# Performance work log

Measured on AMD Instinct MI355X. Metric: run time of the kernel, lower is better.

Reference implementation:

```python
import jax, jax.numpy as jnp
import numpy as np

TEMPERATURE = 0.07
EPS = 1e-12  # F.normalize eps


def _construct_labels(visual_ids, anchor_idx):
    # Faithful vectorization of the original order-dependent double loop:
    # for i < B-1: final write to labels[i] comes from pair (i, B-1)
    #   -> 1 iff ids[i]==anchor_id and ids[B-1]==anchor_id, else 0
    # for i == B-1: final write comes from pair (B-2, B-1)
    #   -> 1 iff ids[B-1]==anchor_id and ids[B-2]==anchor_id, else 0
    B = visual_ids.shape[0]
    anchor_id = visual_ids[anchor_idx]
    same = visual_ids == anchor_id  # [B] bool
    labels = jnp.where(same & same[B - 1], 1, 0).astype(jnp.int32)
    labels = labels.at[B - 1].set((same[B - 1] & same[B - 2]).astype(jnp.int32))
    return labels


def setup_inputs() -> dict:
    key = jax.random.key(0)
    k1, k2 = jax.random.split(key)
    visual_feat = jax.random.normal(k1, (8192, 512), dtype=jnp.float32)
    visual_ids = jax.random.randint(k2, (8192,), 0, 1024, dtype=jnp.int64 if jax.config.jax_enable_x64 else jnp.int32)
    anchor_idx = 3
    return {"visual_feat": visual_feat, "visual_ids": visual_ids, "anchor_idx": anchor_idx}


def reference(visual_feat, visual_ids, anchor_idx):
    # L2 normalize rows (F.normalize: x / max(||x||, eps))
    norm = jnp.sqrt(jnp.sum(visual_feat * visual_feat, axis=1, keepdims=True))
    f = visual_feat / jnp.maximum(norm, EPS)
    sim = jnp.matmul(f, f.T) / TEMPERATURE  # [B, B]
    labels = _construct_labels(visual_ids, anchor_idx)  # [B] int in {0,1}
    logp = jax.nn.log_softmax(sim, axis=-1)  # [B, B]
    picked = jnp.take_along_axis(logp, labels[:, None], axis=1)[:, 0]
    loss = -jnp.mean(picked)
    return loss
```

## Files before the change

kernel.cpp:

```cpp
#include <hip/hip_runtime.h>


typedef int i32x8 __attribute__((ext_vector_type(8)));
typedef float f32x4 __attribute__((ext_vector_type(4)));

#define B_N 8192
#define D_K 512
#define ROWB 512
#define INVT 14.285714285714286f
#define SCALE_LOG2 20.609929155556622f

#if defined(__has_builtin) && __has_builtin(__builtin_amdgcn_exp2f)
#define FAST_EXP2(x) __builtin_amdgcn_exp2f(x)
#else
#define FAST_EXP2(x) exp2f(x)
#endif

union FragU {
  int4 h[2];
  i32x8 v;
};

static __device__ __forceinline__ void load16_to_lds(const void* g, void* l) {
  __builtin_amdgcn_global_load_lds(
      (const __attribute__((address_space(1))) unsigned int*)g,
      (__attribute__((address_space(3))) unsigned int*)l, 16, 0, 0);
}

static __device__ __forceinline__ void bar_nodrain() {
  __builtin_amdgcn_sched_barrier(0);
  asm volatile("" ::: "memory");
  __builtin_amdgcn_s_barrier();
  asm volatile("" ::: "memory");
  __builtin_amdgcn_sched_barrier(0);
}

#define VM_WAIT(N) asm volatile("s_waitcnt vmcnt(" #N ")" ::: "memory")

__global__ __launch_bounds__(256)
void norm_kernel(const float* __restrict__ x,
                 unsigned char* __restrict__ fQ,
                 float* __restrict__ Z) {
  const int row = blockIdx.x * 4 + (threadIdx.x >> 6);
  const int lane = threadIdx.x & 63;
  const float4* xr = (const float4*)(x + (size_t)row * D_K);
  float4 a = xr[2 * lane];
  float4 b = xr[2 * lane + 1];
  float s = a.x * a.x + a.y * a.y + a.z * a.z + a.w * a.w +
            b.x * b.x + b.y * b.y + b.z * b.z + b.w * b.w;
#pragma unroll
  for (int off = 1; off < 64; off <<= 1) s += __shfl_xor(s, off);
  const float inv = 1.0f / fmaxf(sqrtf(s), 1e-12f);
  int lo = 0, hi = 0;
  lo = __builtin_amdgcn_cvt_pk_fp8_f32(a.x * inv, a.y * inv, lo, false);
  lo = __builtin_amdgcn_cvt_pk_fp8_f32(a.z * inv, a.w * inv, lo, true);
  hi = __builtin_amdgcn_cvt_pk_fp8_f32(b.x * inv, b.y * inv, hi, false);
  hi = __builtin_amdgcn_cvt_pk_fp8_f32(b.z * inv, b.w * inv, hi, true);
  int2 p; p.x = lo; p.y = hi;
  ((int2*)(fQ + (size_t)row * ROWB))[lane] = p;
  if (lane == 0) Z[row] = 0.0f;
}

__global__ __launch_bounds__(256, 2)
void sim_kernel(const unsigned char* __restrict__ fQ,
                float* __restrict__ Z, float* __restrict__ T01,
                float* __restrict__ D) {
  __shared__ unsigned char ldsA[3 * 128 * 128];
  __shared__ unsigned char ldsB[2 * 128 * 128];

  const int tid = threadIdx.x;
  const int lane = tid & 63;
  const int w = tid >> 6;
  const int wm = w & 1;
  const int wn = w >> 1;
  const int bx = blockIdx.x, by = blockIdx.y;
  const int b = by & 7;
  const int I = (by < 8) ? bx : (63 - bx);
  const int Jfirst = I + ((b - I) & 7);
  if (Jfirst > 63) return;
  const int I0 = I * 128;

  const int srow = lane >> 3;
  const int sb = lane & 7;
  const int su = sb ^ srow;
  const int sg = 2 * (su & 3) + (su >> 2);
  const size_t sOff = (size_t)srow * ROWB + sg * 16;

  const int fr = lane & 15;
  const int q = lane >> 4;
  const int swz = fr & 7;

  const int raRow = (wm * 64 + fr) * 128;
  const int rbRow = (wn * 64 + fr) * 128;
  const int off0 = (q ^ swz) * 16;
  const int off1 = ((q + 4) ^ swz) * 16;

  FragU u3[4];
  {
    const unsigned char* aReg =
        fQ + (size_t)(I0 + wm * 64 + fr) * ROWB + 3 * 128 + q * 32;
#pragma unroll
    for (int m = 0; m < 4; ++m) {
      const unsigned char* p = aReg + (size_t)(m * 16) * ROWB;
      u3[m].h[0] = *(const int4*)(p);
      u3[m].h[1] = *(const int4*)(p + 16);
    }
  }
#pragma unroll
  for (int m = 0; m < 4; ++m) asm volatile("" ::"v"(u3[m].v));

#pragma unroll
  for (int kk = 0; kk < 3; ++kk) {
    const unsigned char* gA = fQ + (size_t)(I0 + w * 32) * ROWB + kk * 128 + sOff;
    unsigned char* lA = ldsA + kk * (128 * 128) + (w * 32) * 128;
#pragma unroll
    for (int rr = 0; rr < 32; rr += 8)
      load16_to_lds(gA + (size_t)rr * ROWB, lA + rr * 128);
  }

  int curOff = 0;
  {
    const unsigned char* gB =
        fQ + (size_t)(Jfirst * 128 + w * 32) * ROWB + sOff;
    unsigned char* lB = ldsB + (w * 32) * 128;
#pragma unroll
    for (int rr = 0; rr < 32; rr += 8)
      load16_to_lds(gB + (size_t)rr * ROWB, lB + rr * 128);
  }

  float Zp[4][4];
#pragma unroll
  for (int m = 0; m < 4; ++m)
#pragma unroll
    for (int r = 0; r < 4; ++r) Zp[m][r] = 0.0f;

  f32x4 acc[4][4];

#pragma unroll 1
  for (int J = Jfirst; J < 64; J += 8) {
    const int J0 = J * 128;
#pragma unroll
    for (int m = 0; m < 4; ++m)
#pragma unroll
      for (int n = 0; n < 4; ++n) acc[m][n] = (f32x4){0.f, 0.f, 0.f, 0.f};

#pragma unroll 1
    for (int kk = 0; kk < 3; ++kk) {
      {
        const unsigned char* gB =
            fQ + (size_t)(J0 + w * 32) * ROWB + (kk + 1) * 128 + sOff;
        unsigned char* lB = ldsB + (curOff ^ 16384) + (w * 32) * 128;
#pragma unroll
        for (int rr = 0; rr < 32; rr += 8)
          load16_to_lds(gB + (size_t)rr * ROWB, lB + rr * 128);
      }
      VM_WAIT(4);
      bar_nodrain();

      const unsigned char* raBase = ldsA + kk * (128 * 128) + raRow;
      const unsigned char* rbBase = ldsB + curOff + rbRow;
      i32x8 bv[4];
#pragma unroll
      for (int n = 0; n < 4; ++n) {
        const unsigned char* rb = rbBase + n * 16 * 128;
        FragU u;
        u.h[0] = *(const int4*)(rb + off0);
        u.h[1] = *(const int4*)(rb + off1);
        bv[n] = u.v;
      }
      __builtin_amdgcn_s_setprio(1);
#pragma unroll
      for (int mh = 0; mh < 2; ++mh) {
        i32x8 av[2];
#pragma unroll
        for (int m = 0; m < 2; ++m) {
          const unsigned char* ra = raBase + (mh * 2 + m) * 16 * 128;
          FragU u;
          u.h[0] = *(const int4*)(ra + off0);
          u.h[1] = *(const int4*)(ra + off1);
          av[m] = u.v;
        }
#pragma unroll
        for (int m = 0; m < 2; ++m)
#pragma unroll
          for (int n = 0; n < 4; ++n)
            acc[mh * 2 + m][n] = __builtin_amdgcn_mfma_scale_f32_16x16x128_f8f6f4(
                av[m], bv[n], acc[mh * 2 + m][n], 0, 0, 0, 127, 0, 127);
      }
      __builtin_amdgcn_s_setprio(0);
      bar_nodrain();
      curOff ^= 16384;
    }

    const bool hasNext = (J + 8) < 64;
    if (hasNext) {
      const unsigned char* gB =
          fQ + (size_t)((J + 8) * 128 + w * 32) * ROWB + sOff;
      unsigned char* lB = ldsB + (curOff ^ 16384) + (w * 32) * 128;
#pragma unroll
      for (int rr = 0; rr < 32; rr += 8)
        load16_to_lds(gB + (size_t)rr * ROWB, lB + rr * 128);
      VM_WAIT(4);
    } else {
      VM_WAIT(0);
    }
    bar_nodrain();
    {
      const unsigned char* rbBase = ldsB + curOff + rbRow;
      i32x8 bv[4];
#pragma unroll
      for (int n = 0; n < 4; ++n) {
        const unsigned char* rb = rbBase + n * 16 * 128;
        FragU u;
        u.h[0] = *(const int4*)(rb + off0);
        u.h[1] = *(const int4*)(rb + off1);
        bv[n] = u.v;
      }
      __builtin_amdgcn_s_setprio(1);
#pragma unroll
      for (int m = 0; m < 4; ++m)
#pragma unroll
        for (int n = 0; n < 4; ++n)
          acc[m][n] = __builtin_amdgcn_mfma_scale_f32_16x16x128_f8f6f4(
              u3[m].v, bv[n], acc[m][n], 0, 0, 0, 127, 0, 127);
      __builtin_amdgcn_s_setprio(0);
    }
    curOff ^= 16384;

    if (I == 0 && wm == 0) {
      if (q == 0) {
#pragma unroll
        for (int n = 0; n < 4; ++n) {
          const int col = J0 + wn * 64 + n * 16 + fr;
          T01[col * 2 + 0] = acc[0][n][0] * INVT;
          T01[col * 2 + 1] = acc[0][n][1] * INVT;
        }
      }
    }

    if (J == I) {
#pragma unroll
      for (int m = 0; m < 4; ++m)
#pragma unroll
        for (int n = 0; n < 4; ++n) {
          const int col = J0 + wn * 64 + n * 16 + fr;
#pragma unroll
          for (int r = 0; r < 4; ++r) {
            const int row = I0 + wm * 64 + m * 16 + q * 4 + r;
            if (row == col) D[row] = acc[m][n][r];
          }
        }
    }

    const bool offd = (J != I);
#pragma unroll
    for (int n = 0; n < 4; ++n) {
      float cs = 0.0f;
#pragma unroll
      for (int m = 0; m < 4; ++m)
#pragma unroll
        for (int r = 0; r < 4; ++r) {
          const float e = FAST_EXP2((acc[m][n][r] - 1.0f) * SCALE_LOG2);
          Zp[m][r] += e;
          cs += e;
        }
      if (offd) {
        cs += __shfl_xor(cs, 16);
        cs += __shfl_xor(cs, 32);
        if (q == 0) atomicAdd(&Z[J0 + wn * 64 + n * 16 + fr], cs);
      }
    }

    bar_nodrain();
  }

#pragma unroll
  for (int m = 0; m < 4; ++m)
#pragma unroll
    for (int r = 0; r < 4; ++r) {
      float v = Zp[m][r];
      v += __shfl_xor(v, 1);
      v += __shfl_xor(v, 2);
      v += __shfl_xor(v, 4);
      v += __shfl_xor(v, 8);
      if (fr == 0) atomicAdd(&Z[I0 + wm * 64 + m * 16 + q * 4 + r], v);
    }
}

__global__ __launch_bounds__(1024)
void finalize_kernel(const float* __restrict__ Z,
                     const float* __restrict__ T01,
                     const float* __restrict__ D,
                     const int* __restrict__ ids,
                     const int* __restrict__ anchor,
                     float* __restrict__ out) {
  __shared__ float red[1024];
  const int t = threadIdx.x;
  const int anchor_id = ids[anchor[0]];
  const int sameLast = (ids[B_N - 1] == anchor_id);
  const int samePrev = (ids[B_N - 2] == anchor_id);
  int i[8], id[8];
  float z[8], d[8], t0[8], t1[8];
#pragma unroll
  for (int u = 0; u < 8; ++u) {
    i[u] = u * 1024 + t;
    z[u] = Z[i[u]];
    d[u] = D[i[u]];
    t0[u] = T01[i[u] * 2 + 0];
    t1[u] = T01[i[u] * 2 + 1];
    id[u] = ids[i[u]];
  }
  float sum = 0.0f;
#pragma unroll
  for (int u = 0; u < 8; ++u) {
    const int same_i = (id[u] == anchor_id);
    const int lab =
        (i[u] < B_N - 1) ? (same_i & sameLast) : (sameLast & samePrev);
    const float tt = lab ? t1[u] : t0[u];
    const float Zc = z[u] - FAST_EXP2((d[u] - 1.0f) * SCALE_LOG2) + 1.0f;
    sum += tt - (INVT + logf(Zc));
  }
  red[t] = sum;
  __syncthreads();
  for (int off = 512; off > 0; off >>= 1) {
    if (t < off) red[t] += red[t + off];
    __syncthreads();
  }
  if (t == 0) out[0] = -red[0] / (float)B_N;
}

extern "C" void kernel_launch(void* const* d_in, const int* in_sizes, int n_in,
                              void* d_out, int out_size, void* d_ws, size_t ws_size,
                              hipStream_t stream) {
  const float* x = (const float*)d_in[0];
  const int* ids = (const int*)d_in[1];
  const int* anchor = (const int*)d_in[2];
  float* out = (float*)d_out;

  unsigned char* fQ = (unsigned char*)d_ws;
  float* Z = (float*)((char*)d_ws + (size_t)B_N * ROWB);
  float* T01 = Z + B_N;
  float* D = T01 + 2 * B_N;

  norm_kernel<<<B_N / 4, 256, 0, stream>>>(x, fQ, Z);
  sim_kernel<<<dim3(32, 16), 256, 0, stream>>>(fQ, Z, T01, D);
  finalize_kernel<<<1, 1024, 0, stream>>>(Z, T01, D, ids, anchor, out);
}
```

Before: 107.4 us.

## Keep three A K-slices in registers and shrink A LDS to one slice

Three of the four 128-wide K slices of the A tile now live in registers for the whole block, and only K slice 0 is staged in LDS. This cuts LDS from 80KB to 48KB and removes the A-side LDS reads for those slices. The k-loop is unrolled, and B fragments are now loaded per column and consumed right away instead of being buffered as a full set of four. The cost is much higher VGPR pressure (48 extra 8-dword fragments per thread), which risks spills or lower occupancy under launch_bounds(256,2).

```diff
diff --git a/kernel.cpp b/kernel.cpp
--- a/kernel.cpp
+++ b/kernel.cpp
@@ -65,7 +65,7 @@
 void sim_kernel(const unsigned char* __restrict__ fQ,
                 float* __restrict__ Z, float* __restrict__ T01,
                 float* __restrict__ D) {
-  __shared__ unsigned char ldsA[3 * 128 * 128];
+  __shared__ unsigned char ldsA0[128 * 128];
   __shared__ unsigned char ldsB[2 * 128 * 128];
 
   const int tid = threadIdx.x;
@@ -95,24 +95,28 @@
   const int off0 = (q ^ swz) * 16;
   const int off1 = ((q + 4) ^ swz) * 16;
 
-  FragU u3[4];
+  FragU uA[3][4];
   {
-    const unsigned char* aReg =
-        fQ + (size_t)(I0 + wm * 64 + fr) * ROWB + 3 * 128 + q * 32;
-#pragma unroll
-    for (int m = 0; m < 4; ++m) {
-      const unsigned char* p = aReg + (size_t)(m * 16) * ROWB;
-      u3[m].h[0] = *(const int4*)(p);
-      u3[m].h[1] = *(const int4*)(p + 16);
-    }
-  }
-#pragma unroll
-  for (int m = 0; m < 4; ++m) asm volatile("" ::"v"(u3[m].v));
-
-#pragma unroll
-  for (int kk = 0; kk < 3; ++kk) {
-    const unsigned char* gA = fQ + (size_t)(I0 + w * 32) * ROWB + kk * 128 + sOff;
-    unsigned char* lA = ldsA + kk * (128 * 128) + (w * 32) * 128;
+    const unsigned char* aBase =
+        fQ + (size_t)(I0 + wm * 64 + fr) * ROWB + q * 32;
+#pragma unroll
+    for (int k = 0; k < 3; ++k) {
+#pragma unroll
+      for (int m = 0; m < 4; ++m) {
+        const unsigned char* p = aBase + (size_t)(m * 16) * ROWB + (k + 1) * 128;
+        uA[k][m].h[0] = *(const int4*)(p);
+        uA[k][m].h[1] = *(const int4*)(p + 16);
+      }
+    }
+  }
+#pragma unroll
+  for (int k = 0; k < 3; ++k)
+#pragma unroll
+    for (int m = 0; m < 4; ++m) asm volatile("" ::"v"(uA[k][m].v));
+
+  {
+    const unsigned char* gA = fQ + (size_t)(I0 + w * 32) * ROWB + sOff;
+    unsigned char* lA = ldsA0 + (w * 32) * 128;
 #pragma unroll
     for (int rr = 0; rr < 32; rr += 8)
       load16_to_lds(gA + (size_t)rr * ROWB, lA + rr * 128);
@@ -144,11 +148,10 @@
 #pragma unroll
       for (int n = 0; n < 4; ++n) acc[m][n] = (f32x4){0.f, 0.f, 0.f, 0.f};
 
-#pragma unroll 1
-    for (int kk = 0; kk < 3; ++kk) {
+    {
       {
         const unsigned char* gB =
-            fQ + (size_t)(J0 + w * 32) * ROWB + (kk + 1) * 128 + sOff;
+            fQ + (size_t)(J0 + w * 32) * ROWB + 1 * 128 + sOff;
         unsigned char* lB = ldsB + (curOff ^ 16384) + (w * 32) * 128;
 #pragma unroll
         for (int rr = 0; rr < 32; rr += 8)
@@ -157,35 +160,58 @@
       VM_WAIT(4);
       bar_nodrain();
 
-      const unsigned char* raBase = ldsA + kk * (128 * 128) + raRow;
       const unsigned char* rbBase = ldsB + curOff + rbRow;
-      i32x8 bv[4];
+      i32x8 av[4];
+#pragma unroll
+      for (int m = 0; m < 4; ++m) {
+        const unsigned char* ra = ldsA0 + raRow + m * 16 * 128;
+        FragU u;
+        u.h[0] = *(const int4*)(ra + off0);
+        u.h[1] = *(const int4*)(ra + off1);
+        av[m] = u.v;
+      }
+      __builtin_amdgcn_s_setprio(1);
 #pragma unroll
       for (int n = 0; n < 4; ++n) {
         const unsigned char* rb = rbBase + n * 16 * 128;
-        FragU u;
-        u.h[0] = *(const int4*)(rb + off0);
-        u.h[1] = *(const int4*)(rb + off1);
-        bv[n] = u.v;
-      }
+        FragU ub;
+        ub.h[0] = *(const int4*)(rb + off0);
+        ub.h[1] = *(const int4*)(rb + off1);
+#pragma unroll
+        for (int m = 0; m < 4; ++m)
+          acc[m][n] = __builtin_amdgcn_mfma_scale_f32_16x16x128_f8f6f4(
+              av[m], ub.v, acc[m][n], 0, 0, 0, 127, 0, 127);
+      }
+      __builtin_amdgcn_s_setprio(0);
+      bar_nodrain();
+      curOff ^= 16384;
+    }
+
+#pragma unroll
+    for (int k = 0; k < 2; ++k) {
+      {
+        const unsigned char* gB =
+            fQ + (size_t)(J0 + w * 32) * ROWB + (k + 2) * 128 + sOff;
+        unsigned char* lB = ldsB + (curOff ^ 16384) + (w * 32) * 128;
+#pragma unroll
+        for (int rr = 0; rr < 32; rr += 8)
+          load16_to_lds(gB + (size_t)rr * ROWB, lB + rr * 128);
+      }
+      VM_WAIT(4);
+      bar_nodrain();
+
+      const unsigned char* rbBase = ldsB + curOff + rbRow;
       __builtin_amdgcn_s_setprio(1);
 #pragma unroll
-      for (int mh = 0; mh < 2; ++mh) {
-        i32x8 av[2];
-#pragma unroll
-        for (int m = 0; m < 2; ++m) {
-          const unsigned char* ra = raBase + (mh * 2 + m) * 16 * 128;
-          FragU u;
-          u.h[0] = *(const int4*)(ra + off0);
-          u.h[1] = *(const int4*)(ra + off1);
-          av[m] = u.v;
-        }
-#pragma unroll
-        for (int m = 0; m < 2; ++m)
-#pragma unroll
-          for (int n = 0; n < 4; ++n)
-            acc[mh * 2 + m][n] = __builtin_amdgcn_mfma_scale_f32_16x16x128_f8f6f4(
-                av[m], bv[n], acc[mh * 2 + m][n], 0, 0, 0, 127, 0, 127);
+      for (int n = 0; n < 4; ++n) {
+        const unsigned char* rb = rbBase + n * 16 * 128;
+        FragU ub;
+        ub.h[0] = *(const int4*)(rb + off0);
+        ub.h[1] = *(const int4*)(rb + off1);
+#pragma unroll
+        for (int m = 0; m < 4; ++m)
+          acc[m][n] = __builtin_amdgcn_mfma_scale_f32_16x16x128_f8f6f4(
+              uA[k][m].v, ub.v, acc[m][n], 0, 0, 0, 127, 0, 127);
       }
       __builtin_amdgcn_s_setprio(0);
       bar_nodrain();
@@ -207,22 +233,18 @@
     bar_nodrain();
     {
       const unsigned char* rbBase = ldsB + curOff + rbRow;
-      i32x8 bv[4];
+      __builtin_amdgcn_s_setprio(1);
 #pragma unroll
       for (int n = 0; n < 4; ++n) {
         const unsigned char* rb = rbBase + n * 16 * 128;
-        FragU u;
-        u.h[0] = *(const int4*)(rb + off0);
-        u.h[1] = *(const int4*)(rb + off1);
-        bv[n] = u.v;
-      }
-      __builtin_amdgcn_s_setprio(1);
-#pragma unroll
-      for (int m = 0; m < 4; ++m)
-#pragma unroll
-        for (int n = 0; n < 4; ++n)
+        FragU ub;
+        ub.h[0] = *(const int4*)(rb + off0);
+        ub.h[1] = *(const int4*)(rb + off1);
+#pragma unroll
+        for (int m = 0; m < 4; ++m)
           acc[m][n] = __builtin_amdgcn_mfma_scale_f32_16x16x128_f8f6f4(
-              u3[m].v, bv[n], acc[m][n], 0, 0, 0, 127, 0, 127);
+              uA[2][m].v, ub.v, acc[m][n], 0, 0, 0, 127, 0, 127);
+      }
       __builtin_amdgcn_s_setprio(0);
     }
     curOff ^= 16384;
```

Measured after the change: 187.7 us. +74.7%, slower.
